# Kernel optimization log

Hardware: AMD Instinct MI355X
Metric: run time of the kernel (lower is better)

Reference implementation:

```python
import jax, jax.numpy as jnp
import numpy as np
import math

SR = 96000.0
FRAME = 2048          # FRAME_SIZE
NB = 16               # N_BIQUADS
B, F = 16, 128        # batch, n_frames
N = F * FRAME         # n_samples (divisible by FRAME)

GAIN_RANGE = (-24.0, 24.0)
BROADBAND = (-60.0, 0.0)
Q_RANGE = (0.5, 16.0)
HPF_R = (20.0, 500.0)
LPF_R = (5000.0, 20000.0)
SHELF_R = (50.0, 16000.0)
PEAK_R = (100.0, 15000.0)


def _denorm_freq(n, r):
    lo, hi = math.log(r[0]), math.log(r[1])
    return jnp.exp(lo + n * (hi - lo))


def _denorm_gain(n, r):
    return r[0] + n * (r[1] - r[0])


def _denorm_q(n):
    lo, hi = math.log(Q_RANGE[0]), math.log(Q_RANGE[1])
    return jnp.exp(lo + n * (hi - lo))


def _norm(b0, b1, b2, a0, a1, a2):
    return b0 / a0, b1 / a0, b2 / a0, a1 / a0, a2 / a0


def _hp(fc, Q):
    w0 = 2 * math.pi * fc / SR
    al = jnp.sin(w0) / (2 * Q)
    c = jnp.cos(w0)
    return _norm((1 + c) / 2, -(1 + c), (1 + c) / 2, 1 + al, -2 * c, 1 - al)


def _lp(fc, Q):
    w0 = 2 * math.pi * fc / SR
    al = jnp.sin(w0) / (2 * Q)
    c = jnp.cos(w0)
    return _norm((1 - c) / 2, 1 - c, (1 - c) / 2, 1 + al, -2 * c, 1 - al)


def _peak(fc, g_db, Q):
    A = jnp.power(10.0, g_db / 40.0)
    w0 = 2 * math.pi * fc / SR
    al = jnp.sin(w0) / (2 * Q)
    c = jnp.cos(w0)
    return _norm(1 + al * A, -2 * c, 1 - al * A, 1 + al / A, -2 * c, 1 - al / A)


def _lowshelf(fc, g_db, Q):
    A = jnp.power(10.0, g_db / 40.0)
    w0 = 2 * math.pi * fc / SR
    al = jnp.sin(w0) / (2 * Q)
    c = jnp.cos(w0)
    sA = jnp.sqrt(A)
    b0 = A * (A + 1 - (A - 1) * c + 2 * sA * al)
    b1 = 2 * A * (A - 1 - (A + 1) * c)
    b2 = A * (A + 1 - (A - 1) * c - 2 * sA * al)
    a0 = A + 1 + (A - 1) * c + 2 * sA * al
    a1 = -2 * (A - 1 + (A + 1) * c)
    a2 = A + 1 + (A - 1) * c - 2 * sA * al
    return _norm(b0, b1, b2, a0, a1, a2)


def _highshelf(fc, g_db, Q):
    A = jnp.power(10.0, g_db / 40.0)
    w0 = 2 * math.pi * fc / SR
    al = jnp.sin(w0) / (2 * Q)
    c = jnp.cos(w0)
    sA = jnp.sqrt(A)
    b0 = A * (A + 1 + (A - 1) * c + 2 * sA * al)
    b1 = -2 * A * (A - 1 + (A + 1) * c)
    b2 = A * (A + 1 + (A - 1) * c - 2 * sA * al)
    a0 = A + 1 - (A - 1) * c + 2 * sA * al
    a1 = 2 * (A - 1 - (A + 1) * c)
    a2 = A + 1 - (A - 1) * c - 2 * sA * al
    return _norm(b0, b1, b2, a0, a1, a2)


def _forward(audio, params):
    b, n = audio.shape
    f = n // FRAME
    fp = params.shape[2]
    # per-audio-frame parameter index: min(frame_idx, n_frames_params-1)
    idx = jnp.minimum(jnp.arange(f), fp - 1)
    p = params[:, :, idx]                       # (B, 50, F)
    bq = p[:, : NB * 3, :].reshape(b, NB, 3, f)  # (B, 16, 3, F)
    in_g = jnp.power(10.0, _denorm_gain(p[:, -2, :], BROADBAND) / 20.0)   # (B,F)
    out_g = jnp.power(10.0, _denorm_gain(p[:, -1, :], BROADBAND) / 20.0)  # (B,F)

    x = audio.reshape(b, f, FRAME) * in_g[:, :, None]

    # per-stage normalized coefficients, each (B, F)
    coefs = []
    for i in range(NB):
        fn, gn, qn = bq[:, i, 0], bq[:, i, 1], bq[:, i, 2]
        Q = _denorm_q(qn)
        if i == 0:                      # BIQUAD_HPF
            c = _hp(_denorm_freq(fn, HPF_R), Q)
        elif i == NB - 1:               # BIQUAD_LPF
            c = _lp(_denorm_freq(fn, LPF_R), Q)
        elif i == 1:                    # BIQUAD_LOW_SHELF
            c = _lowshelf(_denorm_freq(fn, SHELF_R), _denorm_gain(gn, GAIN_RANGE), Q)
        elif i == NB - 2:               # BIQUAD_HIGH_SHELF
            c = _highshelf(_denorm_freq(fn, SHELF_R), _denorm_gain(gn, GAIN_RANGE), Q)
        else:                           # peaking EQ
            c = _peak(_denorm_freq(fn, PEAK_R), _denorm_gain(gn, GAIN_RANGE), Q)
        coefs.append(jnp.stack(c))      # (5, B, F)
    C = jnp.stack(coefs).reshape(NB, 5, b * f)  # (16, 5, B*F)

    # each (batch, frame) lane filters independently with zero initial state
    xt = x.reshape(b * f, FRAME).T              # (T, B*F)

    def step(s, v):
        # s: (16, 2, B*F) DF2T states; v: (B*F,) cascade input
        new_s = []
        for i in range(NB):
            b0, b1, b2, a1, a2 = C[i, 0], C[i, 1], C[i, 2], C[i, 3], C[i, 4]
            y = b0 * v + s[i, 0]
            s1 = b1 * v - a1 * y + s[i, 1]
            s2 = b2 * v - a2 * y
            new_s.append(jnp.stack([s1, s2]))
            v = y
        return jnp.stack(new_s), v

    s0 = jnp.zeros((NB, 2, b * f), dtype=audio.dtype)
    _, ys = jax.lax.scan(step, s0, xt)          # (T, B*F)

    y = ys.T.reshape(b, f, FRAME) * out_g[:, :, None]
    return y.reshape(b, n)


def setup_inputs() -> dict:
    key = jax.random.key(0)
    k1, k2 = jax.random.split(key)
    audio = jax.random.normal(k1, (B, N), dtype=jnp.float32)
    params = jax.random.uniform(k2, (B, 50, F), dtype=jnp.float32)
    return {"audio": audio, "params": params}


def reference(audio, params):
    return _forward(audio, params)
```

## Files before the change

### kernel.cpp

```cpp
#include <hip/hip_runtime.h>
#include <math.h>

namespace {

constexpr int kNB    = 16;
constexpr int kFrame = 2048;
constexpr int kHalf  = 16;
constexpr int kWPB   = 4;

typedef float f32x2 __attribute__((ext_vector_type(2)));

__device__ inline f32x2 pk_fma(f32x2 a, f32x2 b, f32x2 c) {
    f32x2 d;
    asm("v_pk_fma_f32 %0, %1, %2, %3" : "=v"(d) : "v"(a), "v"(b), "v"(c));
    return d;
}
__device__ inline f32x2 pk_mul(f32x2 a, f32x2 b) {
    f32x2 d;
    asm("v_pk_mul_f32 %0, %1, %2" : "=v"(d) : "v"(a), "v"(b));
    return d;
}
__device__ inline f32x2 pk_add(f32x2 a, f32x2 b) {
    f32x2 d;
    asm("v_pk_add_f32 %0, %1, %2" : "=v"(d) : "v"(a), "v"(b));
    return d;
}

__global__ __launch_bounds__(256)
void biquad_chain_kernel(const float* __restrict__ audio,
                         const float* __restrict__ params,
                         float* __restrict__ out)
{
    __shared__ float sC[kWPB][kNB][5];
    __shared__ float sLvl[kWPB][kNB][7][3];

    const int tid  = threadIdx.x;
    const int wv   = tid >> 6;
    const int lane = tid & 63;
    const int ch   = blockIdx.x * kWPB + wv;
    const int bb   = ch >> 7;
    const int ff   = ch & 127;

    const float* pb = params + (size_t)bb * (50 * 128) + ff;

    if (lane < kNB) {
        const int band = lane;
        const double fn = (double)pb[(band * 3 + 0) * 128];
        const double gn = (double)pb[(band * 3 + 1) * 128];
        const double qn = (double)pb[(band * 3 + 2) * 128];
        const double PI   = 3.14159265358979323846;
        const double LN10 = 2.302585092994046;

        const bool isHP = (band == 0), isLP = (band == kNB - 1);
        const bool isShelf = (band == 1) || (band == kNB - 2);
        const double flo = isHP ? 2.995732273553991
                        : isLP ? 8.517193191416238
                        : isShelf ? 3.912023005428146
                        : 4.605170185988092;
        const double fsp = isHP ? 3.2188758248682006
                        : isLP ? 1.3862943611198906
                        : isShelf ? 5.768320995793772
                        : 5.0106352940962555;

        const double Q  = exp(-0.6931471805599453 + qn * 3.4657359027997265);
        const double fc = exp(flo + fn * fsp);
        const double w0 = (2.0 * PI / 96000.0) * fc;
        const double sw = sin(w0);
        const double cw = cos(w0);
        const double al = sw / (2.0 * Q);
        const double gdb = (isHP || isLP) ? 0.0 : (-24.0 + gn * 48.0);
        const double A   = exp(gdb * (LN10 / 40.0));
        const double sA  = sqrt(A);
        const double ge = isHP ? (-60.0 + (double)pb[48 * 128] * 60.0) * (LN10 / 20.0)
                        : isLP ? (-60.0 + (double)pb[49 * 128] * 60.0) * (LN10 / 20.0)
                        : 0.0;
        const double gm = exp(ge);

        double b0, b1, b2, a0, a1, a2;
        if (isHP) {
            b0 = (1.0 + cw) * 0.5; b1 = -(1.0 + cw); b2 = (1.0 + cw) * 0.5;
            a0 = 1.0 + al; a1 = -2.0 * cw; a2 = 1.0 - al;
        } else if (isLP) {
            b0 = (1.0 - cw) * 0.5; b1 = 1.0 - cw; b2 = (1.0 - cw) * 0.5;
            a0 = 1.0 + al; a1 = -2.0 * cw; a2 = 1.0 - al;
        } else if (band == 1) {
            const double s2 = 2.0 * sA * al;
            b0 = A * ((A + 1.0) - (A - 1.0) * cw + s2);
            b1 = 2.0 * A * ((A - 1.0) - (A + 1.0) * cw);
            b2 = A * ((A + 1.0) - (A - 1.0) * cw - s2);
            a0 = (A + 1.0) + (A - 1.0) * cw + s2;
            a1 = -2.0 * ((A - 1.0) + (A + 1.0) * cw);
            a2 = (A + 1.0) + (A - 1.0) * cw - s2;
        } else if (band == kNB - 2) {
            const double s2 = 2.0 * sA * al;
            b0 = A * ((A + 1.0) + (A - 1.0) * cw + s2);
            b1 = -2.0 * A * ((A - 1.0) + (A + 1.0) * cw);
            b2 = A * ((A + 1.0) + (A - 1.0) * cw - s2);
            a0 = (A + 1.0) - (A - 1.0) * cw + s2;
            a1 = 2.0 * ((A - 1.0) - (A + 1.0) * cw);
            a2 = (A + 1.0) - (A - 1.0) * cw - s2;
        } else {
            b0 = 1.0 + al * A; b1 = -2.0 * cw; b2 = 1.0 - al * A;
            a0 = 1.0 + al / A; a1 = -2.0 * cw; a2 = 1.0 - al / A;
        }
        const double inv  = 1.0 / a0;
        const double binv = inv * gm;
        b0 *= binv; b1 *= binv; b2 *= binv; a1 *= inv; a2 *= inv;

        sC[wv][band][0] = (float)b0;
        sC[wv][band][1] = (float)b1;
        sC[wv][band][2] = (float)b2;
        sC[wv][band][3] = (float)(-a1);
        sC[wv][band][4] = (float)(-a2);

        double ap = 1.0, bp = 0.0;
        #pragma unroll
        for (int s = 0; s < 10; ++s) {
            const double an = ap * (2.0 * bp - a1 * ap);
            const double bn = bp * bp - a2 * (ap * ap);
            ap = an; bp = bn;
            if (s >= 3) {
                const int L = s - 3;
                sLvl[wv][band][L][0] = (float)ap;
                sLvl[wv][band][L][1] = (float)bp;
                sLvl[wv][band][L][2] = (float)(-a2 * ap);
            }
        }
    }
    __syncthreads();

    f32x2 X[kHalf];
    {
        const float4* ap = reinterpret_cast<const float4*>(
            audio + (size_t)ch * kFrame + lane * 32);
        #pragma unroll
        for (int k = 0; k < 4; ++k) {
            const float4 va = ap[k];
            const float4 vb = ap[k + 4];
            X[4 * k + 0] = f32x2{va.x, vb.x};
            X[4 * k + 1] = f32x2{va.y, vb.y};
            X[4 * k + 2] = f32x2{va.z, vb.z};
            X[4 * k + 3] = f32x2{va.w, vb.w};
        }
    }

    for (int band = 0; band < kNB; ++band) {
        const float b0  = sC[wv][band][0];
        const float b1  = sC[wv][band][1];
        const float b2  = sC[wv][band][2];
        const float na1 = sC[wv][band][3];
        const float na2 = sC[wv][band][4];
        const f32x2 b0p  = {b0, b0},  b1p = {b1, b1}, b2p = {b2, b2};
        const f32x2 na1p = {na1, na1}, na2p = {na2, na2};

        f32x2 s1 = {0.f, 0.f}, s2 = {0.f, 0.f};
        #pragma unroll
        for (int t = 0; t < kHalf; ++t) {
            const f32x2 xv = X[t];
            const f32x2 y  = pk_fma(b0p, xv, s1);
            const f32x2 tm = pk_fma(b1p, xv, s2);
            s2 = pk_fma(na2p, y, pk_mul(b2p, xv));
            s1 = pk_fma(na1p, y, tm);
            X[t] = y;
        }

        const float al16 = sLvl[wv][band][0][0];
        const float be16 = sLvl[wv][band][0][1];
        const float ga16 = sLvl[wv][band][0][2];
        const float wf = fmaf(na1, s1.x, s2.x);
        const float d0 = fmaf(al16, wf, fmaf(be16, s1.x, s1.y));
        const float d1 = fmaf(ga16, s1.x, fmaf(be16, s2.x, s2.y));

        float v0, v1;
        {
            const float e0 = __shfl_up(d0, 1);
            const float e1 = __shfl_up(d1, 1);
            v0 = (lane == 0) ? 0.f : e0;
            v1 = (lane == 0) ? 0.f : e1;
        }
        #pragma unroll
        for (int j = 0; j < 6; ++j) {
            const int s = 1 << j;
            const float alpha = sLvl[wv][band][j + 1][0];
            const float beta  = sLvl[wv][band][j + 1][1];
            const float gamma = sLvl[wv][band][j + 1][2];
            float t0 = __shfl_up(v0, (unsigned)s);
            float t1 = __shfl_up(v1, (unsigned)s);
            const bool ok = (lane >= s);
            t0 = ok ? t0 : 0.f;
            t1 = ok ? t1 : 0.f;
            const float w = fmaf(na1, t0, t1);
            v0 = fmaf(alpha, w,  fmaf(beta, t0, v0));
            v1 = fmaf(gamma, t0, fmaf(beta, t1, v1));
        }

        const float wr  = fmaf(na1, v0, v1);
        const float uB0 = fmaf(al16, wr, fmaf(be16, v0, s1.x));
        const float uB1 = fmaf(ga16, v0, fmaf(be16, v1, s2.x));

        f32x2 w0 = {v0, uB0}, w1 = {v1, uB1};
        #pragma unroll
        for (int t = 0; t < kHalf; ++t) {
            const f32x2 c = w0;
            X[t] = pk_add(X[t], c);
            w0 = pk_fma(na1p, c, w1);
            w1 = pk_mul(na2p, c);
        }
    }

    {
        float4* op = reinterpret_cast<float4*>(out + (size_t)ch * kFrame + lane * 32);
        #pragma unroll
        for (int k = 0; k < 4; ++k) {
            op[k]     = float4{X[4 * k + 0].x, X[4 * k + 1].x, X[4 * k + 2].x, X[4 * k + 3].x};
            op[k + 4] = float4{X[4 * k + 0].y, X[4 * k + 1].y, X[4 * k + 2].y, X[4 * k + 3].y};
        }
    }
}

}

extern "C" void kernel_launch(void* const* d_in, const int* in_sizes, int n_in,
                              void* d_out, int out_size, void* d_ws, size_t ws_size,
                              hipStream_t stream)
{
    (void)d_ws; (void)ws_size; (void)n_in; (void)in_sizes;
    const float* audio  = (const float*)d_in[0];
    const float* params = (const float*)d_in[1];
    float* outp = (float*)d_out;

    const int channels = out_size / kFrame;
    const int blocks   = channels / kWPB;

    hipLaunchKernelGGL(biquad_chain_kernel, dim3(blocks), dim3(256), 0, stream,
                       audio, params, outp);
}
```

Baseline: 30.01 us.

## Split each channel across two wavefronts with cross-wave state carry via LDS

Each 2048-sample channel is now handled by two wavefronts (one per half), so each lane holds 16 samples instead of 32, which shortens the serial per-lane recurrence and doubles the thread count (2048 channels → 1024 blocks of 4 waves). The scan-level coefficients are recomputed for 8-sample blocks. The first half's end state is passed through shared memory, and the second half propagates it to each lane using binary-decomposed powers of the transition. This adds a __syncthreads per band (16 per kernel) and some extra per-lane math in exchange for more parallelism and lower register pressure.

```diff
diff --git a/kernel.cpp b/kernel.cpp
--- a/kernel.cpp
+++ b/kernel.cpp
@@ -5,8 +5,7 @@
 
 constexpr int kNB    = 16;
 constexpr int kFrame = 2048;
-constexpr int kHalf  = 16;
-constexpr int kWPB   = 4;
+constexpr int kSub   = 8;
 
 typedef float f32x2 __attribute__((ext_vector_type(2)));
 
@@ -26,24 +25,27 @@
     return d;
 }
 
-__global__ __launch_bounds__(256)
+__global__ __launch_bounds__(256, 4)
 void biquad_chain_kernel(const float* __restrict__ audio,
                          const float* __restrict__ params,
                          float* __restrict__ out)
 {
-    __shared__ float sC[kWPB][kNB][5];
-    __shared__ float sLvl[kWPB][kNB][7][3];
+    __shared__ float sC[2][kNB][8];
+    __shared__ float sLvl[2][kNB][7][4];
+    __shared__ float sD[2][2][2];
 
     const int tid  = threadIdx.x;
-    const int wv   = tid >> 6;
+    const int w    = tid >> 6;
     const int lane = tid & 63;
-    const int ch   = blockIdx.x * kWPB + wv;
+    const int c    = w >> 1;
+    const int h    = w & 1;
+    const int ch   = blockIdx.x * 2 + c;
     const int bb   = ch >> 7;
     const int ff   = ch & 127;
 
     const float* pb = params + (size_t)bb * (50 * 128) + ff;
 
-    if (lane < kNB) {
+    if (h == 0 && lane < kNB) {
         const int band = lane;
         const double fn = (double)pb[(band * 3 + 0) * 128];
         const double gn = (double)pb[(band * 3 + 1) * 128];
@@ -107,36 +109,37 @@
         const double binv = inv * gm;
         b0 *= binv; b1 *= binv; b2 *= binv; a1 *= inv; a2 *= inv;
 
-        sC[wv][band][0] = (float)b0;
-        sC[wv][band][1] = (float)b1;
-        sC[wv][band][2] = (float)b2;
-        sC[wv][band][3] = (float)(-a1);
-        sC[wv][band][4] = (float)(-a2);
+        sC[c][band][0] = (float)b0;
+        sC[c][band][1] = (float)b1;
+        sC[c][band][2] = (float)b2;
+        sC[c][band][3] = (float)(-a1);
+        sC[c][band][4] = (float)(-a2);
 
         double ap = 1.0, bp = 0.0;
         #pragma unroll
-        for (int s = 0; s < 10; ++s) {
+        for (int s = 0; s < 9; ++s) {
             const double an = ap * (2.0 * bp - a1 * ap);
             const double bn = bp * bp - a2 * (ap * ap);
             ap = an; bp = bn;
-            if (s >= 3) {
-                const int L = s - 3;
-                sLvl[wv][band][L][0] = (float)ap;
-                sLvl[wv][band][L][1] = (float)bp;
-                sLvl[wv][band][L][2] = (float)(-a2 * ap);
+            if (s >= 2) {
+                const int L = s - 2;
+                sLvl[c][band][L][0] = (float)ap;
+                sLvl[c][band][L][1] = (float)bp;
+                sLvl[c][band][L][2] = (float)(-a2 * ap);
+                sLvl[c][band][L][3] = 0.f;
             }
         }
     }
     __syncthreads();
 
-    f32x2 X[kHalf];
+    f32x2 X[kSub];
     {
         const float4* ap = reinterpret_cast<const float4*>(
-            audio + (size_t)ch * kFrame + lane * 32);
-        #pragma unroll
-        for (int k = 0; k < 4; ++k) {
+            audio + (size_t)ch * kFrame + h * 1024 + lane * 16);
+        #pragma unroll
+        for (int k = 0; k < 2; ++k) {
             const float4 va = ap[k];
-            const float4 vb = ap[k + 4];
+            const float4 vb = ap[k + 2];
             X[4 * k + 0] = f32x2{va.x, vb.x};
             X[4 * k + 1] = f32x2{va.y, vb.y};
             X[4 * k + 2] = f32x2{va.z, vb.z};
@@ -145,17 +148,18 @@
     }
 
     for (int band = 0; band < kNB; ++band) {
-        const float b0  = sC[wv][band][0];
-        const float b1  = sC[wv][band][1];
-        const float b2  = sC[wv][band][2];
-        const float na1 = sC[wv][band][3];
-        const float na2 = sC[wv][band][4];
+        const float b0  = sC[c][band][0];
+        const float b1  = sC[c][band][1];
+        const float b2  = sC[c][band][2];
+        const float na1 = sC[c][band][3];
+        const float na2 = sC[c][band][4];
+        const float* L  = &sLvl[c][band][0][0];
         const f32x2 b0p  = {b0, b0},  b1p = {b1, b1}, b2p = {b2, b2};
         const f32x2 na1p = {na1, na1}, na2p = {na2, na2};
 
         f32x2 s1 = {0.f, 0.f}, s2 = {0.f, 0.f};
         #pragma unroll
-        for (int t = 0; t < kHalf; ++t) {
+        for (int t = 0; t < kSub; ++t) {
             const f32x2 xv = X[t];
             const f32x2 y  = pk_fma(b0p, xv, s1);
             const f32x2 tm = pk_fma(b1p, xv, s2);
@@ -164,12 +168,10 @@
             X[t] = y;
         }
 
-        const float al16 = sLvl[wv][band][0][0];
-        const float be16 = sLvl[wv][band][0][1];
-        const float ga16 = sLvl[wv][band][0][2];
+        const float al8 = L[0], be8 = L[1], ga8 = L[2];
         const float wf = fmaf(na1, s1.x, s2.x);
-        const float d0 = fmaf(al16, wf, fmaf(be16, s1.x, s1.y));
-        const float d1 = fmaf(ga16, s1.x, fmaf(be16, s2.x, s2.y));
+        const float d0 = fmaf(al8, wf, fmaf(be8, s1.x, s1.y));
+        const float d1 = fmaf(ga8, s1.x, fmaf(be8, s2.x, s2.y));
 
         float v0, v1;
         {
@@ -181,39 +183,71 @@
         #pragma unroll
         for (int j = 0; j < 6; ++j) {
             const int s = 1 << j;
-            const float alpha = sLvl[wv][band][j + 1][0];
-            const float beta  = sLvl[wv][band][j + 1][1];
-            const float gamma = sLvl[wv][band][j + 1][2];
+            const float alj = L[4 * (j + 1) + 0];
+            const float bej = L[4 * (j + 1) + 1];
+            const float gaj = L[4 * (j + 1) + 2];
             float t0 = __shfl_up(v0, (unsigned)s);
             float t1 = __shfl_up(v1, (unsigned)s);
             const bool ok = (lane >= s);
             t0 = ok ? t0 : 0.f;
             t1 = ok ? t1 : 0.f;
-            const float w = fmaf(na1, t0, t1);
-            v0 = fmaf(alpha, w,  fmaf(beta, t0, v0));
-            v1 = fmaf(gamma, t0, fmaf(beta, t1, v1));
+            const float wj = fmaf(na1, t0, t1);
+            v0 = fmaf(alj, wj, fmaf(bej, t0, v0));
+            v1 = fmaf(gaj, t0, fmaf(bej, t1, v1));
+        }
+
+        if (h == 0) {
+            const float al16 = L[4], be16 = L[5], ga16 = L[6];
+            const float wD = fmaf(na1, v0, v1);
+            const float D0 = fmaf(al16, wD, fmaf(be16, v0, d0));
+            const float D1 = fmaf(ga16, v0, fmaf(be16, v1, d1));
+            if (lane == 63) {
+                sD[c][band & 1][0] = D0;
+                sD[c][band & 1][1] = D1;
+            }
+        }
+        __syncthreads();
+
+        if (h == 1) {
+            float g0 = sD[c][band & 1][0];
+            float g1 = sD[c][band & 1][1];
+            #pragma unroll
+            for (int j = 0; j < 6; ++j) {
+                const float alj = L[4 * (j + 1) + 0];
+                const float bej = L[4 * (j + 1) + 1];
+                const float gaj = L[4 * (j + 1) + 2];
+                const float wj = fmaf(na1, g0, g1);
+                const float m0 = fmaf(alj, wj, bej * g0);
+                const float m1 = fmaf(gaj, g0, bej * g1);
+                const bool bit = ((lane >> j) & 1) != 0;
+                g0 = bit ? m0 : g0;
+                g1 = bit ? m1 : g1;
+            }
+            v0 += g0;
+            v1 += g1;
         }
 
         const float wr  = fmaf(na1, v0, v1);
-        const float uB0 = fmaf(al16, wr, fmaf(be16, v0, s1.x));
-        const float uB1 = fmaf(ga16, v0, fmaf(be16, v1, s2.x));
+        const float uB0 = fmaf(al8, wr, fmaf(be8, v0, s1.x));
+        const float uB1 = fmaf(ga8, v0, fmaf(be8, v1, s2.x));
 
         f32x2 w0 = {v0, uB0}, w1 = {v1, uB1};
         #pragma unroll
-        for (int t = 0; t < kHalf; ++t) {
-            const f32x2 c = w0;
-            X[t] = pk_add(X[t], c);
-            w0 = pk_fma(na1p, c, w1);
-            w1 = pk_mul(na2p, c);
+        for (int t = 0; t < kSub; ++t) {
+            const f32x2 cc = w0;
+            X[t] = pk_add(X[t], cc);
+            w0 = pk_fma(na1p, cc, w1);
+            w1 = pk_mul(na2p, cc);
         }
     }
 
     {
-        float4* op = reinterpret_cast<float4*>(out + (size_t)ch * kFrame + lane * 32);
-        #pragma unroll
-        for (int k = 0; k < 4; ++k) {
+        float4* op = reinterpret_cast<float4*>(
+            out + (size_t)ch * kFrame + h * 1024 + lane * 16);
+        #pragma unroll
+        for (int k = 0; k < 2; ++k) {
             op[k]     = float4{X[4 * k + 0].x, X[4 * k + 1].x, X[4 * k + 2].x, X[4 * k + 3].x};
-            op[k + 4] = float4{X[4 * k + 0].y, X[4 * k + 1].y, X[4 * k + 2].y, X[4 * k + 3].y};
+            op[k + 2] = float4{X[4 * k + 0].y, X[4 * k + 1].y, X[4 * k + 2].y, X[4 * k + 3].y};
         }
     }
 }
@@ -230,7 +264,7 @@
     float* outp = (float*)d_out;
 
     const int channels = out_size / kFrame;
-    const int blocks   = channels / kWPB;
+    const int blocks   = channels / 2;
 
     hipLaunchKernelGGL(biquad_chain_kernel, dim3(blocks), dim3(256), 0, stream,
                        audio, params, outp);
```

Measured after the change: 37.49 us. 24.9% more time.

## Replace shuffle-based scan with DPP row shifts and broadcast levels, one wave per block

Applied to the files above, without the earlier changes.

Replaces the ds_bpermute-based __shfl_up Kogge-Stone scan over the 64 lanes with DPP row_shr operations for shifts 1-8, then row_bcast15/31 for the cross-row steps. Those broadcast steps need per-lane transition powers, so a power table is precomputed from all 64 lanes in parallel. Blocks shrink from four waves to one, and the coefficient setup now spreads across all lanes instead of 16. This is meant to cut the LDS-shuffle latency on the serial scan path, at the cost of a larger per-band power table and more double-precision setup per lane.

```diff
diff --git a/kernel.cpp b/kernel.cpp
--- a/kernel.cpp
+++ b/kernel.cpp
@@ -6,7 +6,6 @@
 constexpr int kNB    = 16;
 constexpr int kFrame = 2048;
 constexpr int kHalf  = 16;
-constexpr int kWPB   = 4;
 
 typedef float f32x2 __attribute__((ext_vector_type(2)));
 
@@ -26,25 +25,39 @@
     return d;
 }
 
-__global__ __launch_bounds__(256)
+template <int CTRL>
+__device__ inline float dpp_f(float v) {
+    return __int_as_float(
+        __builtin_amdgcn_update_dpp(0, __float_as_int(v), CTRL, 0xF, 0xF, true));
+}
+
+template <int CTRL>
+__device__ inline void ks_level(float& v0, float& v1, const float4 M, const float na1) {
+    const float t0 = dpp_f<CTRL>(v0);
+    const float t1 = dpp_f<CTRL>(v1);
+    const float w  = fmaf(na1, t0, t1);
+    v0 = fmaf(M.x, w,  fmaf(M.y, t0, v0));
+    v1 = fmaf(M.z, t0, fmaf(M.y, t1, v1));
+}
+
+__global__ __launch_bounds__(64)
 void biquad_chain_kernel(const float* __restrict__ audio,
                          const float* __restrict__ params,
                          float* __restrict__ out)
 {
-    __shared__ float sC[kWPB][kNB][5];
-    __shared__ float sLvl[kWPB][kNB][7][3];
-
-    const int tid  = threadIdx.x;
-    const int wv   = tid >> 6;
-    const int lane = tid & 63;
-    const int ch   = blockIdx.x * kWPB + wv;
+    __shared__ float4 sK[kNB][2];
+    __shared__ float4 powT[kNB][33];
+
+    const int lane = threadIdx.x & 63;
+    const int ch   = blockIdx.x;
     const int bb   = ch >> 7;
     const int ff   = ch & 127;
 
     const float* pb = params + (size_t)bb * (50 * 128) + ff;
 
-    if (lane < kNB) {
-        const int band = lane;
+    {
+        const int band = lane & 15;
+        const int part = lane >> 4;
         const double fn = (double)pb[(band * 3 + 0) * 128];
         const double gn = (double)pb[(band * 3 + 1) * 128];
         const double qn = (double)pb[(band * 3 + 2) * 128];
@@ -107,24 +120,45 @@
         const double binv = inv * gm;
         b0 *= binv; b1 *= binv; b2 *= binv; a1 *= inv; a2 *= inv;
 
-        sC[wv][band][0] = (float)b0;
-        sC[wv][band][1] = (float)b1;
-        sC[wv][band][2] = (float)b2;
-        sC[wv][band][3] = (float)(-a1);
-        sC[wv][band][4] = (float)(-a2);
-
-        double ap = 1.0, bp = 0.0;
-        #pragma unroll
-        for (int s = 0; s < 10; ++s) {
-            const double an = ap * (2.0 * bp - a1 * ap);
-            const double bn = bp * bp - a2 * (ap * ap);
-            ap = an; bp = bn;
-            if (s >= 3) {
-                const int L = s - 3;
-                sLvl[wv][band][L][0] = (float)ap;
-                sLvl[wv][band][L][1] = (float)bp;
-                sLvl[wv][band][L][2] = (float)(-a2 * ap);
-            }
+        double alc = 1.0, bec = 0.0;
+        double al16 = 0, be16 = 0, al32 = 0, be32 = 0;
+        double al256 = 0, be256 = 0, al512 = 0, be512 = 0;
+        #pragma unroll
+        for (int k = 1; k <= 9; ++k) {
+            const double a_ = alc, b_ = bec;
+            alc = a_ * (2.0 * b_ - a1 * a_);
+            bec = b_ * b_ - a2 * (a_ * a_);
+            if (k == 4) { al16 = alc; be16 = bec; }
+            if (k == 5) { al32 = alc; be32 = bec; }
+            if (k == 8) { al256 = alc; be256 = bec; }
+            if (k == 9) { al512 = alc; be512 = bec; }
+        }
+        auto cmp = [&](double alx, double bex, double aly, double bey,
+                       double& alo, double& beo) {
+            const double p = alx * aly;
+            alo = alx * bey + bex * aly - a1 * p;
+            beo = bex * bey - a2 * p;
+        };
+
+        double Sa, Sb;
+        if (part == 0)      { Sa = al32; Sb = be32; }
+        else if (part == 1) { cmp(al256, be256, al32, be32, Sa, Sb); }
+        else if (part == 2) { cmp(al512, be512, al32, be32, Sa, Sb); }
+        else { double ta, tb; cmp(al512, be512, al256, be256, ta, tb);
+               cmp(ta, tb, al32, be32, Sa, Sb); }
+
+        #pragma unroll
+        for (int j = 0; j < 8; ++j) {
+            powT[band][8 * part + j] =
+                float4{(float)Sa, (float)Sb, (float)(-a2 * Sa), 0.f};
+            double na, nb;
+            cmp(Sa, Sb, al32, be32, na, nb);
+            Sa = na; Sb = nb;
+        }
+        if (part == 0) {
+            sK[band][0] = float4{(float)b0, (float)b1, (float)b2, (float)(-a1)};
+            sK[band][1] = float4{(float)(-a2), (float)al16, (float)be16,
+                                 (float)(-a2 * al16)};
         }
     }
     __syncthreads();
@@ -145,11 +179,17 @@
     }
 
     for (int band = 0; band < kNB; ++band) {
-        const float b0  = sC[wv][band][0];
-        const float b1  = sC[wv][band][1];
-        const float b2  = sC[wv][band][2];
-        const float na1 = sC[wv][band][3];
-        const float na2 = sC[wv][band][4];
+        const float4 k0 = sK[band][0];
+        const float4 k1 = sK[band][1];
+        const float4 P1 = powT[band][0];
+        const float4 P2 = powT[band][1];
+        const float4 P4 = powT[band][3];
+        const float4 P8 = powT[band][7];
+        const float4 Pme = powT[band][lane & 15];
+        const float4 Qme = powT[band][lane & 31];
+
+        const float b0 = k0.x, b1 = k0.y, b2 = k0.z, na1 = k0.w;
+        const float na2 = k1.x, al16 = k1.y, be16 = k1.z, ga16 = k1.w;
         const f32x2 b0p  = {b0, b0},  b1p = {b1, b1}, b2p = {b2, b2};
         const f32x2 na1p = {na1, na1}, na2p = {na2, na2};
 
@@ -164,34 +204,35 @@
             X[t] = y;
         }
 
-        const float al16 = sLvl[wv][band][0][0];
-        const float be16 = sLvl[wv][band][0][1];
-        const float ga16 = sLvl[wv][band][0][2];
         const float wf = fmaf(na1, s1.x, s2.x);
         const float d0 = fmaf(al16, wf, fmaf(be16, s1.x, s1.y));
         const float d1 = fmaf(ga16, s1.x, fmaf(be16, s2.x, s2.y));
 
-        float v0, v1;
+        float v0 = dpp_f<0x138>(d0);
+        float v1 = dpp_f<0x138>(d1);
+        ks_level<0x111>(v0, v1, P1, na1);
+        ks_level<0x112>(v0, v1, P2, na1);
+        ks_level<0x114>(v0, v1, P4, na1);
+        ks_level<0x118>(v0, v1, P8, na1);
         {
-            const float e0 = __shfl_up(d0, 1);
-            const float e1 = __shfl_up(d1, 1);
-            v0 = (lane == 0) ? 0.f : e0;
-            v1 = (lane == 0) ? 0.f : e1;
-        }
-        #pragma unroll
-        for (int j = 0; j < 6; ++j) {
-            const int s = 1 << j;
-            const float alpha = sLvl[wv][band][j + 1][0];
-            const float beta  = sLvl[wv][band][j + 1][1];
-            const float gamma = sLvl[wv][band][j + 1][2];
-            float t0 = __shfl_up(v0, (unsigned)s);
-            float t1 = __shfl_up(v1, (unsigned)s);
-            const bool ok = (lane >= s);
-            t0 = ok ? t0 : 0.f;
-            t1 = ok ? t1 : 0.f;
+            float t0 = dpp_f<0x142>(v0);
+            float t1 = dpp_f<0x142>(v1);
+            const bool g = (lane & 16) != 0;
+            t0 = g ? t0 : 0.f;
+            t1 = g ? t1 : 0.f;
             const float w = fmaf(na1, t0, t1);
-            v0 = fmaf(alpha, w,  fmaf(beta, t0, v0));
-            v1 = fmaf(gamma, t0, fmaf(beta, t1, v1));
+            v0 = fmaf(Pme.x, w,  fmaf(Pme.y, t0, v0));
+            v1 = fmaf(Pme.z, t0, fmaf(Pme.y, t1, v1));
+        }
+        {
+            float t0 = dpp_f<0x143>(v0);
+            float t1 = dpp_f<0x143>(v1);
+            const bool g = lane >= 32;
+            t0 = g ? t0 : 0.f;
+            t1 = g ? t1 : 0.f;
+            const float w = fmaf(na1, t0, t1);
+            v0 = fmaf(Qme.x, w,  fmaf(Qme.y, t0, v0));
+            v1 = fmaf(Qme.z, t0, fmaf(Qme.y, t1, v1));
         }
 
         const float wr  = fmaf(na1, v0, v1);
@@ -230,8 +271,6 @@
     float* outp = (float*)d_out;
 
     const int channels = out_size / kFrame;
-    const int blocks   = channels / kWPB;
-
-    hipLaunchKernelGGL(biquad_chain_kernel, dim3(blocks), dim3(256), 0, stream,
+    hipLaunchKernelGGL(biquad_chain_kernel, dim3(channels), dim3(64), 0, stream,
                        audio, params, outp);
 }
```

After: 26.45 us, median of 2. 11.9% less time.
